# Performance work log

Measured on AMD Instinct MI355X. Metric: run time of the kernel, lower is better.

## Reference

```python
import jax, jax.numpy as jnp
import numpy as np

D_IN = 1024
D_OUT = 1024


def setup_inputs() -> dict:
    key = jax.random.key(0)
    ks = jax.random.split(key, 7)
    B, S = 4, 2048
    x = jax.random.normal(ks[0], (B, S, D_IN), dtype=jnp.float32)
    s = 1.0 / np.sqrt(D_IN)
    Wq = jax.random.uniform(ks[1], (D_IN, D_OUT), jnp.float32, -s, s)
    Wk = jax.random.uniform(ks[2], (D_IN, D_OUT), jnp.float32, -s, s)
    Wv = jax.random.uniform(ks[3], (D_IN, D_OUT), jnp.float32, -s, s)
    bq = jax.random.uniform(ks[4], (D_OUT,), jnp.float32, -s, s)
    bk = jax.random.uniform(ks[5], (D_OUT,), jnp.float32, -s, s)
    bv = jax.random.uniform(ks[6], (D_OUT,), jnp.float32, -s, s)
    return {"x": x, "Wq": Wq, "Wk": Wk, "Wv": Wv, "bq": bq, "bk": bk, "bv": bv}


def reference(x, Wq, Wk, Wv, bq, bk, bv):
    # x: [B, S, d_in]
    B, S, _ = x.shape
    q = x @ Wq + bq            # [B, S, d_out]
    k = x @ Wk + bk
    v = x @ Wv + bv
    scale = 1.0 / jnp.sqrt(jnp.asarray(q.shape[-1], q.dtype))
    scores = jnp.einsum('bqd,bkd->bqk', q, k)  # [B, S, S]
    causal = jnp.tril(jnp.ones((S, S), dtype=bool))
    scores = jnp.where(causal, scores, -jnp.inf)
    attn = jax.nn.softmax(scores * scale, axis=-1)
    return jnp.einsum('bqk,bkd->bqd', attn, v)
```

## Files before the change

### kernel.cpp

```cpp
#include <hip/hip_runtime.h>
#include <cstdint>

#define DEV __device__ __forceinline__

typedef __attribute__((ext_vector_type(4))) float f32x4;
typedef __attribute__((ext_vector_type(8))) short short8;
typedef __attribute__((ext_vector_type(4))) unsigned short u16x4;

constexpr int BS  = 4;
constexpr int SEQ = 2048;

DEV ushort f2b(float f){
  uint32_t u = __builtin_bit_cast(uint32_t, f);
  u += 0x7fffu + ((u >> 16) & 1u);
  return (ushort)(u >> 16);
}
DEV float b2f(ushort h){
  uint32_t u = (uint32_t)h << 16;
  return __builtin_bit_cast(float, u);
}

DEV void gload_lds16(const void* g, void* l){
  __builtin_amdgcn_global_load_lds(
      (const __attribute__((address_space(1))) unsigned int*)g,
      (__attribute__((address_space(3))) unsigned int*)l, 16, 0, 0);
}

#define BAR()    __builtin_amdgcn_s_barrier()
#define PRIO(x)  __builtin_amdgcn_s_setprio(x)
#define SCHEDB() __builtin_amdgcn_sched_barrier(0)
#define LGKM0()  asm volatile("s_waitcnt lgkmcnt(0)" ::: "memory")
#define WAITV(n) asm volatile("s_waitcnt vmcnt(" #n ")" ::: "memory")

__global__ __launch_bounds__(256) void convert_f2b8(const float* __restrict__ src,
                                                    ushort* __restrict__ dst){
  long i = (long)blockIdx.x * 256 + threadIdx.x;
  const f32x4* s4 = (const f32x4*)src;
  f32x4 a = s4[i*2], b = s4[i*2+1];
  short8 o;
  o[0]=(short)f2b(a[0]); o[1]=(short)f2b(a[1]); o[2]=(short)f2b(a[2]); o[3]=(short)f2b(a[3]);
  o[4]=(short)f2b(b[0]); o[5]=(short)f2b(b[1]); o[6]=(short)f2b(b[2]); o[7]=(short)f2b(b[3]);
  ((short8*)dst)[i] = o;
}

__global__ __launch_bounds__(256) void transpose_f2b(const float* __restrict__ src,
                                                     ushort* __restrict__ dst,
                                                     int R, int C){
  __shared__ float t[32][33];
  int c0 = blockIdx.x * 32, r0 = blockIdx.y * 32;
  int tx = threadIdx.x, ty = threadIdx.y;
  #pragma unroll
  for (int k=0;k<4;k++) t[ty+k*8][tx] = src[(long)(r0+ty+k*8)*C + c0+tx];
  __syncthreads();
  #pragma unroll
  for (int k=0;k<4;k++) dst[(long)(c0+ty+k*8)*R + r0+tx] = f2b(t[tx][ty+k*8]);
}

__global__ __launch_bounds__(256) void transpose_b2b(const ushort* __restrict__ src,
                                                     ushort* __restrict__ dst,
                                                     int R, int C){
  __shared__ ushort t[32][33];
  int c0 = blockIdx.x * 32, r0 = blockIdx.y * 32;
  int tx = threadIdx.x, ty = threadIdx.y;
  #pragma unroll
  for (int k=0;k<4;k++) t[ty+k*8][tx] = src[(long)(r0+ty+k*8)*C + c0+tx];
  __syncthreads();
  #pragma unroll
  for (int k=0;k<4;k++) dst[(long)(c0+ty+k*8)*R + r0+tx] = t[tx][ty+k*8];
}

struct GArgs {
  const ushort* A;  long lda; long aBS;
  const ushort* Bm; long ldb; long bBS;
  void* C;          long ldc; long cBS;
  const float* b0; const float* b1; const float* b2;
  int K;
};

template<int MODE>
__global__ __launch_bounds__(512, 2) void ring256(GArgs g){
  extern __shared__ char sm[];
  int m0, n0, z = 0;
  if (MODE == 0){
    const int fid = blockIdx.x;
    const int xcd = fid & 7, j = fid >> 3;
    m0 = (xcd * 4 + (j & 3)) * 256;
    n0 = (j >> 2) * 256;
  } else {
    m0 = blockIdx.x * 256; n0 = blockIdx.y * 256; z = blockIdx.z;
    if (n0 > m0) return;
  }
  const int tid = threadIdx.x;
  const int wid = tid >> 6, lane = tid & 63;
  const int wr = wid >> 2, wc = wid & 3;
  const int lr = lane & 15, lk = lane >> 4;

  const char* Ab = (const char*)(g.A  + (long)z * g.aBS);
  const char* Bb = (const char*)(g.Bm + (long)z * g.bBS);
  const long lda2 = g.lda * 2, ldb2 = g.ldb * 2;
  const int sr  = tid >> 2;
  const int scb = ((tid & 3) << 4) ^ (((sr >> 3) & 1) << 5);
  const char* aR0 = Ab + (long)(m0       + sr)*lda2 + scb;
  const char* aR1 = Ab + (long)(m0 + 128 + sr)*lda2 + scb;
  const char* bR0 = Bb + (long)(n0       + sr)*ldb2 + scb;
  const char* bR1 = Bb + (long)(n0 + 128 + sr)*ldb2 + scb;
  const int dst = tid << 4;

  int aoff[8], boff[4];
  #pragma unroll
  for (int m=0;m<8;m++){
    int r = wr*128 + m*16 + lr;
    aoff[m] = r*64 + ((lk*16) ^ (((r>>3)&1)<<5));
  }
  #pragma unroll
  for (int n=0;n<4;n++){
    int r = wc*64 + n*16 + lr;
    boff[n] = 16384 + r*64 + ((lk*16) ^ (((r>>3)&1)<<5));
  }

  f32x4 acc[8][4];
  #pragma unroll
  for (int m=0;m<8;m++)
    #pragma unroll
    for (int n=0;n<4;n++) acc[m][n] = f32x4{0.f,0.f,0.f,0.f};

  const int NT = g.K >> 5;
  gload_lds16(aR0,      sm + dst);
  gload_lds16(aR1,      sm + 8192  + dst);
  gload_lds16(bR0,      sm + 16384 + dst);
  gload_lds16(bR1,      sm + 24576 + dst);
  gload_lds16(aR0 + 64, sm + 32768 + dst);
  gload_lds16(aR1 + 64, sm + 32768 + 8192  + dst);
  gload_lds16(bR0 + 64, sm + 32768 + 16384 + dst);
  gload_lds16(bR1 + 64, sm + 32768 + 24576 + dst);
  WAITV(4); BAR();

  int p = 0;
  for (int t = 0; t < NT; ++t){
    const char* base = sm + p*32768;
    const int t2 = (t+2 < NT) ? t+2 : NT-1;
    const long kB = (long)(t2) << 6;
    int pS = p + 2; if (pS >= 3) pS -= 3;
    char* sb = sm + pS*32768;
    short8 af[4], bf[4];
    gload_lds16(aR0 + kB, sb + dst);
    gload_lds16(aR1 + kB, sb + 8192 + dst);
    #pragma unroll
    for (int n=0;n<4;n++) bf[n] = *(const short8*)(base + boff[n]);
    #pragma unroll
    for (int m=0;m<4;m++) af[m] = *(const short8*)(base + aoff[m]);
    LGKM0(); SCHEDB();
    PRIO(1);
    #pragma unroll
    for (int m=0;m<4;m++)
      #pragma unroll
      for (int n=0;n<4;n++)
        acc[m][n] = __builtin_amdgcn_mfma_f32_16x16x32_bf16(af[m], bf[n], acc[m][n], 0,0,0);
    PRIO(0);
    BAR();
    gload_lds16(bR0 + kB, sb + 16384 + dst);
    gload_lds16(bR1 + kB, sb + 24576 + dst);
    #pragma unroll
    for (int m=0;m<4;m++) af[m] = *(const short8*)(base + aoff[4+m]);
    LGKM0(); SCHEDB();
    PRIO(1);
    #pragma unroll
    for (int m=0;m<4;m++)
      #pragma unroll
      for (int n=0;n<4;n++)
        acc[4+m][n] = __builtin_amdgcn_mfma_f32_16x16x32_bf16(af[m], bf[n], acc[4+m][n], 0,0,0);
    PRIO(0);
    WAITV(4);
    BAR();
    p = (p+1 == 3) ? 0 : p+1;
  }
  WAITV(0);

  if (MODE == 0){
    const int sel = n0 >> 10;
    const float* bp = (sel == 0) ? g.b0 : (sel == 1) ? g.b1 : g.b2;
    ushort* Cq = (ushort*)g.C + (long)sel * 8388608;
    const int nq0 = (n0 & 1023);
    #pragma unroll
    for (int n=0;n<4;n++){
      int colq = nq0 + wc*64 + n*16 + lr;
      float bv = bp[colq];
      #pragma unroll
      for (int m=0;m<8;m++){
        int row0 = m0 + wr*128 + m*16 + lk*4;
        #pragma unroll
        for (int i=0;i<4;i++)
          Cq[(long)(row0+i)*1024 + colq] = f2b(acc[m][n][i] + bv);
      }
    }
  } else {
    ushort* Cs = (ushort*)g.C + (long)z * g.cBS;
    #pragma unroll
    for (int m=0;m<8;m++){
      int row0 = m0 + wr*128 + m*16 + lk*4;
      #pragma unroll
      for (int n=0;n<4;n++){
        int col = n0 + wc*64 + n*16 + lr;
        #pragma unroll
        for (int i=0;i<4;i++)
          Cs[(long)(row0+i)*g.ldc + col] = f2b(acc[m][n][i]);
      }
    }
  }
}

template<int MODE>
__global__ __launch_bounds__(512, 2) void gemmB(GArgs g){
  extern __shared__ char sm[];
  const int m0 = blockIdx.x * 128, n0 = blockIdx.y * 256;
  const int z  = blockIdx.z;
  const int tid = threadIdx.x;
  const int wid = tid >> 6, lane = tid & 63;
  const int wr = wid >> 2, wc = wid & 3;
  const int lr = lane & 15, lk = lane >> 4;
  const int f5 = ((lr >> 3) & 1) << 5;

  const char* Ab = (const char*)(g.A  + (long)z * g.aBS);
  const char* Bb = (const char*)(g.Bm + (long)z * g.bBS);
  const long lda2 = g.lda * 2, ldb2 = g.ldb * 2;
  const int sr  = tid >> 2;
  const int scb = ((lane & 3) << 4) ^ (((sr >> 3) & 1) << 5);
  const char* ar0 = Ab + (long)(m0 + sr)*lda2 + scb;
  const char* br0 = Bb + (long)(n0 + sr      )*ldb2 + scb;
  const char* br1 = Bb + (long)(n0 + 128 + sr)*ldb2 + scb;
  const int dwo = wid << 10;

  auto ST = [&](const char* row, int c, int off, int k0){
    const char* p = row + k0*2;
    char* d = sm + c*49152 + off + dwo;
    gload_lds16(p,      d);
    gload_lds16(p + 64, d + 8192);
  };

  const int aoffs = (wr*64 + lr)*64 + ((lk*16) ^ f5);
  const int boffs = 16384 + (wc>>1)*16384 + ((wc&1)*64 + lr)*64 + ((lk*16) ^ f5);

  f32x4 acc[4][4];
  #pragma unroll
  for (int m=0;m<4;m++)
    #pragma unroll
    for (int n=0;n<4;n++) acc[m][n] = f32x4{0.f,0.f,0.f,0.f};

  const int Keff = m0 + 128;
  const int NT = Keff >> 6;
  ST(ar0, 0, 0, 0);
  ST(br0, 0, 16384, 0); ST(br1, 0, 32768, 0);
  ST(br0, 1, 16384, 64); ST(br1, 1, 32768, 64);
  WAITV(4); BAR();

  for (int t = 0; t < NT; ++t){
    const int c = t & 1;
    const char* base = sm + c*49152;
    const int kA = ((t+1) < NT ? (t+1) : NT-1) << 6;
    const int kB = ((t+2) < NT ? (t+2) : NT-1) << 6;
    short8 bf[4][2], af[2][2];
    ST(ar0, c^1, 0, kA);
    #pragma unroll
    for (int n=0;n<4;n++)
      #pragma unroll
      for (int kk=0;kk<2;kk++)
        bf[n][kk] = *(const short8*)(base + boffs + kk*8192 + n*1024);
    #pragma unroll
    for (int mm=0;mm<2;mm++)
      #pragma unroll
      for (int kk=0;kk<2;kk++)
        af[mm][kk] = *(const short8*)(base + aoffs + kk*8192 + mm*1024);
    LGKM0(); SCHEDB();
    PRIO(1);
    #pragma unroll
    for (int kk=0;kk<2;kk++)
      #pragma unroll
      for (int mm=0;mm<2;mm++)
        #pragma unroll
        for (int n=0;n<4;n++)
          acc[mm][n] = __builtin_amdgcn_mfma_f32_16x16x32_bf16(af[mm][kk], bf[n][kk], acc[mm][n], 0,0,0);
    PRIO(0);
    BAR();
    ST(br0, c, 16384, kB); ST(br1, c, 32768, kB);
    #pragma unroll
    for (int mm=0;mm<2;mm++)
      #pragma unroll
      for (int kk=0;kk<2;kk++)
        af[mm][kk] = *(const short8*)(base + aoffs + kk*8192 + (2+mm)*1024);
    LGKM0(); SCHEDB();
    PRIO(1);
    #pragma unroll
    for (int kk=0;kk<2;kk++)
      #pragma unroll
      for (int mm=0;mm<2;mm++)
        #pragma unroll
        for (int n=0;n<4;n++)
          acc[2+mm][n] = __builtin_amdgcn_mfma_f32_16x16x32_bf16(af[mm][kk], bf[n][kk], acc[2+mm][n], 0,0,0);
    PRIO(0);
    WAITV(4);
    BAR();
  }
  WAITV(0);

  long cz = (long)z * g.cBS;
  #pragma unroll
  for (int m=0;m<4;m++){
    int row0 = m0 + wr*64 + m*16 + lk*4;
    #pragma unroll
    for (int n=0;n<4;n++){
      int col = n0 + wc*64 + n*16 + lr;
      #pragma unroll
      for (int i=0;i<4;i++)
        ((float*)g.C)[cz + (long)(row0+i)*g.ldc + col] = acc[m][n][i];
    }
  }
}

__global__ __launch_bounds__(256) void softmax_causal_b(const ushort* __restrict__ sc,
                                                        ushort* __restrict__ P){
  int row = blockIdx.x & (SEQ-1);
  int b   = blockIdx.x >> 11;
  const short8* srow = (const short8*)(sc + ((long)b*SEQ + row)*(long)SEQ);
  ushort* prow = P + ((long)b*SEQ + row)*(long)SEQ;
  int tid = threadIdx.x;
  int lane = tid & 63, wid = tid >> 6;
  const float scale = 0.03125f;
  float x[8]; float mx = -INFINITY;
  int base = tid * 8;
  if (base <= row){
    short8 v = srow[tid];
    #pragma unroll
    for (int j=0;j<8;j++){
      float t = (base + j <= row) ? b2f((ushort)v[j]) : -INFINITY;
      x[j] = t; mx = fmaxf(mx, t);
    }
  } else {
    #pragma unroll
    for (int j=0;j<8;j++) x[j] = -INFINITY;
  }
  #pragma unroll
  for (int off=1; off<64; off<<=1) mx = fmaxf(mx, __shfl_xor(mx, off));
  __shared__ float rb[8];
  if (lane == 0) rb[wid] = mx;
  __syncthreads();
  mx = fmaxf(fmaxf(rb[0],rb[1]), fmaxf(rb[2],rb[3]));
  float sum = 0.f; float e[8];
  #pragma unroll
  for (int i=0;i<8;i++){ e[i] = __expf((x[i]-mx)*scale); sum += e[i]; }
  #pragma unroll
  for (int off=1; off<64; off<<=1) sum += __shfl_xor(sum, off);
  if (lane == 0) rb[4+wid] = sum;
  __syncthreads();
  sum = (rb[4]+rb[5]) + (rb[6]+rb[7]);
  float inv = 1.0f / sum;
  int wlim = row | 127;
  if (base <= wlim){
    short8 o;
    #pragma unroll
    for (int j=0;j<8;j++) o[j] = (short)f2b(e[j]*inv);
    ((short8*)prow)[tid] = o;
  }
}

extern "C" void kernel_launch(void* const* d_in, const int* in_sizes, int n_in,
                              void* d_out, int out_size, void* d_ws, size_t ws_size,
                              hipStream_t stream){
  const float* x  = (const float*)d_in[0];
  const float* Wq = (const float*)d_in[1];
  const float* Wk = (const float*)d_in[2];
  const float* Wv = (const float*)d_in[3];
  const float* bq = (const float*)d_in[4];
  const float* bk = (const float*)d_in[5];
  const float* bv = (const float*)d_in[6];
  float* out = (float*)d_out;

  const long XB = 0;
  const long WT = 16777216;
  const long QB = 23068672;
  const long VT = 73400320;
  const long SC = 90177536;
  const long NEED = 157286400;
  const long PB = 0;
  if ((long)ws_size < NEED) return;

  char* ws = (char*)d_ws;
  ushort* xb = (ushort*)(ws + XB);
  ushort* wt = (ushort*)(ws + WT);
  ushort* qb = (ushort*)(ws + QB);
  ushort* kb = qb + 8388608;
  ushort* vb = qb + 16777216;
  ushort* vt = (ushort*)(ws + VT);
  ushort* sc = (ushort*)(ws + SC);
  ushort* pb = (ushort*)(ws + PB);

  hipFuncSetAttribute(reinterpret_cast<const void*>(&ring256<0>),
                      hipFuncAttributeMaxDynamicSharedMemorySize, 98304);
  hipFuncSetAttribute(reinterpret_cast<const void*>(&ring256<1>),
                      hipFuncAttributeMaxDynamicSharedMemorySize, 98304);
  hipFuncSetAttribute(reinterpret_cast<const void*>(&gemmB<2>),
                      hipFuncAttributeMaxDynamicSharedMemorySize, 98304);

  dim3 tb(32, 8);

  convert_f2b8<<<4096, 256, 0, stream>>>(x, xb);
  transpose_f2b<<<dim3(32,32), tb, 0, stream>>>(Wq, wt + 0,       1024, 1024);
  transpose_f2b<<<dim3(32,32), tb, 0, stream>>>(Wk, wt + 1048576, 1024, 1024);
  transpose_f2b<<<dim3(32,32), tb, 0, stream>>>(Wv, wt + 2097152, 1024, 1024);

  GArgs pa{};
  pa.A = xb; pa.lda = 1024; pa.aBS = 0;
  pa.Bm = wt; pa.ldb = 1024; pa.bBS = 0;
  pa.C = (void*)qb; pa.ldc = 1024; pa.cBS = 0;
  pa.b0 = bq; pa.b1 = bk; pa.b2 = bv;
  pa.K = 1024;
  ring256<0><<<384, 512, 98304, stream>>>(pa);

  transpose_b2b<<<dim3(32,256), tb, 0, stream>>>(vb, vt, 8192, 1024);

  GArgs sa{};
  sa.A = qb;  sa.lda = 1024; sa.aBS = (long)SEQ*1024;
  sa.Bm = kb; sa.ldb = 1024; sa.bBS = (long)SEQ*1024;
  sa.C = (void*)sc; sa.ldc = SEQ; sa.cBS = (long)SEQ*SEQ;
  sa.b0 = nullptr; sa.b1 = nullptr; sa.b2 = nullptr;
  sa.K = 1024;
  ring256<1><<<dim3(8,8,4), 512, 98304, stream>>>(sa);

  softmax_causal_b<<<BS*SEQ, 256, 0, stream>>>(sc, pb);

  GArgs va{};
  va.A = pb;  va.lda = SEQ;  va.aBS = (long)SEQ*SEQ;
  va.Bm = vt; va.ldb = 8192; va.bBS = SEQ;
  va.C = (void*)out; va.ldc = 1024; va.cBS = (long)SEQ*1024;
  va.b0 = nullptr; va.b1 = nullptr; va.b2 = nullptr;
  va.K = SEQ;
  gemmB<2><<<dim3(16,4,4), 512, 98304, stream>>>(va);
}
```

Baseline: 179.3 us.

## Restructure 256x256 GEMM into 8-phase double-buffered K=64 pipeline

Replaces the triple-buffered K=32 ring GEMM used for QKV projection and QK^T scores with a double-buffered K=64 kernel. Each iteration is split into four interleaved phases, where a quarter of the next tiles' global-to-LDS loads is issued, A fragments are read and MFMAs run. The aim is finer overlap of memory and MFMA work with fewer barriers per unit of K. LDS use rises from 96KB to 128KB per block, which may reduce the number of resident blocks per CU and adds more barriers within each iteration.

Result: no change. 178.8 us (-0.3%).

```diff
diff --git a/kernel.cpp b/kernel.cpp
--- a/kernel.cpp
+++ b/kernel.cpp
@@ -30,6 +30,7 @@
 #define PRIO(x)  __builtin_amdgcn_s_setprio(x)
 #define SCHEDB() __builtin_amdgcn_sched_barrier(0)
 #define LGKM0()  asm volatile("s_waitcnt lgkmcnt(0)" ::: "memory")
+#define LGKM8()  asm volatile("s_waitcnt lgkmcnt(8)" ::: "memory")
 #define WAITV(n) asm volatile("s_waitcnt vmcnt(" #n ")" ::: "memory")
 
 __global__ __launch_bounds__(256) void convert_f2b8(const float* __restrict__ src,
@@ -78,13 +79,13 @@
 };
 
 template<int MODE>
-__global__ __launch_bounds__(512, 2) void ring256(GArgs g){
+__global__ __launch_bounds__(512, 2) void gemm8p(GArgs g){
   extern __shared__ char sm[];
   int m0, n0, z = 0;
   if (MODE == 0){
     const int fid = blockIdx.x;
-    const int xcd = fid & 7, j = fid >> 3;
-    m0 = (xcd * 4 + (j & 3)) * 256;
+    const int j = fid >> 3;
+    m0 = ((fid & 7) * 4 + (j & 3)) * 256;
     n0 = (j >> 2) * 256;
   } else {
     m0 = blockIdx.x * 256; n0 = blockIdx.y * 256; z = blockIdx.z;
@@ -98,119 +99,130 @@
   const char* Ab = (const char*)(g.A  + (long)z * g.aBS);
   const char* Bb = (const char*)(g.Bm + (long)z * g.bBS);
   const long lda2 = g.lda * 2, ldb2 = g.ldb * 2;
-  const int sr  = tid >> 2;
-  const int scb = ((tid & 3) << 4) ^ (((sr >> 3) & 1) << 5);
-  const char* aR0 = Ab + (long)(m0       + sr)*lda2 + scb;
-  const char* aR1 = Ab + (long)(m0 + 128 + sr)*lda2 + scb;
-  const char* bR0 = Bb + (long)(n0       + sr)*ldb2 + scb;
-  const char* bR1 = Bb + (long)(n0 + 128 + sr)*ldb2 + scb;
-  const int dst = tid << 4;
+  const int srow = tid >> 2;
+  const int scol = ((tid & 3) << 4) ^ (((tid >> 5) & 1) << 5);
+  const char* sA = Ab + (long)(m0 + srow) * lda2 + scol;
+  const char* sB = Bb + (long)(n0 + srow) * ldb2 + scol;
+  const int dst16 = tid << 4;
+
+  auto STAGE = [&](int tt, int which){
+    const char* s = (which < 2)
+        ? sA + (long)(which & 1) * 128 * lda2 + (long)tt * 128
+        : sB + (long)(which & 1) * 128 * ldb2 + (long)tt * 128;
+    char* d = sm + (tt & 1) * 65536 + which * 16384 + dst16;
+    gload_lds16(s,      d);
+    gload_lds16(s + 64, d + 8192);
+  };
 
   int aoff[8], boff[4];
   #pragma unroll
-  for (int m=0;m<8;m++){
-    int r = wr*128 + m*16 + lr;
-    aoff[m] = r*64 + ((lk*16) ^ (((r>>3)&1)<<5));
-  }
-  #pragma unroll
-  for (int n=0;n<4;n++){
-    int r = wc*64 + n*16 + lr;
-    boff[n] = 16384 + r*64 + ((lk*16) ^ (((r>>3)&1)<<5));
+  for (int mm = 0; mm < 8; mm++){
+    int r = mm * 16 + lr;
+    aoff[mm] = wr * 16384 + r * 64 + ((lk * 16) ^ (((r >> 3) & 1) << 5));
+  }
+  #pragma unroll
+  for (int nn = 0; nn < 4; nn++){
+    int rb = wc * 64 + nn * 16 + lr;
+    boff[nn] = 32768 + (rb >> 7) * 16384 + (rb & 127) * 64
+             + ((lk * 16) ^ (((rb >> 3) & 1) << 5));
   }
 
   f32x4 acc[8][4];
   #pragma unroll
-  for (int m=0;m<8;m++)
-    #pragma unroll
-    for (int n=0;n<4;n++) acc[m][n] = f32x4{0.f,0.f,0.f,0.f};
-
-  const int NT = g.K >> 5;
-  gload_lds16(aR0,      sm + dst);
-  gload_lds16(aR1,      sm + 8192  + dst);
-  gload_lds16(bR0,      sm + 16384 + dst);
-  gload_lds16(bR1,      sm + 24576 + dst);
-  gload_lds16(aR0 + 64, sm + 32768 + dst);
-  gload_lds16(aR1 + 64, sm + 32768 + 8192  + dst);
-  gload_lds16(bR0 + 64, sm + 32768 + 16384 + dst);
-  gload_lds16(bR1 + 64, sm + 32768 + 24576 + dst);
+  for (int m = 0; m < 8; m++)
+    #pragma unroll
+    for (int n = 0; n < 4; n++) acc[m][n] = f32x4{0.f,0.f,0.f,0.f};
+
+  const int NT = g.K >> 6;
+  STAGE(0,2); STAGE(0,3); STAGE(0,0); STAGE(0,1);
+  STAGE(1,2); STAGE(1,3);
   WAITV(4); BAR();
 
-  int p = 0;
+  short8 af[2][2], bf[4][2];
+
+#define READ_A(MB) \
+    af[0][0] = *(const short8*)(base + aoff[MB]);            \
+    af[0][1] = *(const short8*)(base + aoff[MB] + 8192);     \
+    af[1][0] = *(const short8*)(base + aoff[MB+1]);          \
+    af[1][1] = *(const short8*)(base + aoff[MB+1] + 8192);
+#define MFMA16(MB) \
+    PRIO(1); \
+    _Pragma("unroll") \
+    for (int kk = 0; kk < 2; kk++) \
+      _Pragma("unroll") \
+      for (int mm = 0; mm < 2; mm++) \
+        _Pragma("unroll") \
+        for (int nn = 0; nn < 4; nn++) \
+          acc[MB+mm][nn] = __builtin_amdgcn_mfma_f32_16x16x32_bf16(af[mm][kk], bf[nn][kk], acc[MB+mm][nn], 0,0,0); \
+    PRIO(0);
+
   for (int t = 0; t < NT; ++t){
-    const char* base = sm + p*32768;
-    const int t2 = (t+2 < NT) ? t+2 : NT-1;
-    const long kB = (long)(t2) << 6;
-    int pS = p + 2; if (pS >= 3) pS -= 3;
-    char* sb = sm + pS*32768;
-    short8 af[4], bf[4];
-    gload_lds16(aR0 + kB, sb + dst);
-    gload_lds16(aR1 + kB, sb + 8192 + dst);
-    #pragma unroll
-    for (int n=0;n<4;n++) bf[n] = *(const short8*)(base + boff[n]);
-    #pragma unroll
-    for (int m=0;m<4;m++) af[m] = *(const short8*)(base + aoff[m]);
-    LGKM0(); SCHEDB();
-    PRIO(1);
-    #pragma unroll
-    for (int m=0;m<4;m++)
-      #pragma unroll
-      for (int n=0;n<4;n++)
-        acc[m][n] = __builtin_amdgcn_mfma_f32_16x16x32_bf16(af[m], bf[n], acc[m][n], 0,0,0);
-    PRIO(0);
-    BAR();
-    gload_lds16(bR0 + kB, sb + 16384 + dst);
-    gload_lds16(bR1 + kB, sb + 24576 + dst);
-    #pragma unroll
-    for (int m=0;m<4;m++) af[m] = *(const short8*)(base + aoff[4+m]);
-    LGKM0(); SCHEDB();
-    PRIO(1);
-    #pragma unroll
-    for (int m=0;m<4;m++)
-      #pragma unroll
-      for (int n=0;n<4;n++)
-        acc[4+m][n] = __builtin_amdgcn_mfma_f32_16x16x32_bf16(af[m], bf[n], acc[4+m][n], 0,0,0);
-    PRIO(0);
+    const char* base = sm + (t & 1) * 65536;
+    if (t + 1 < NT) STAGE(t+1, 0);
+    #pragma unroll
+    for (int nn = 0; nn < 4; nn++){
+      bf[nn][0] = *(const short8*)(base + boff[nn]);
+      bf[nn][1] = *(const short8*)(base + boff[nn] + 8192);
+    }
+    READ_A(0);
+    LGKM8();
+    SCHEDB(); BAR(); LGKM0(); SCHEDB();
+    MFMA16(0);
+    SCHEDB(); BAR();
+    if (t + 1 < NT) STAGE(t+1, 1);
+    READ_A(2);
+    SCHEDB(); BAR(); LGKM0(); SCHEDB();
+    MFMA16(2);
+    SCHEDB(); BAR();
+    if (t + 2 < NT) STAGE(t+2, 2);
+    READ_A(4);
+    SCHEDB(); BAR(); LGKM0(); SCHEDB();
+    MFMA16(4);
+    SCHEDB(); BAR();
+    if (t + 2 < NT) STAGE(t+2, 3);
+    READ_A(6);
+    SCHEDB(); BAR(); LGKM0(); SCHEDB();
+    MFMA16(6);
     WAITV(4);
-    BAR();
-    p = (p+1 == 3) ? 0 : p+1;
-  }
-  WAITV(0);
+    SCHEDB(); BAR();
+  }
+#undef READ_A
+#undef MFMA16
 
   if (MODE == 0){
     const int sel = n0 >> 10;
     const float* bp = (sel == 0) ? g.b0 : (sel == 1) ? g.b1 : g.b2;
     ushort* Cq = (ushort*)g.C + (long)sel * 8388608;
-    const int nq0 = (n0 & 1023);
-    #pragma unroll
-    for (int n=0;n<4;n++){
-      int colq = nq0 + wc*64 + n*16 + lr;
+    const int nq0 = n0 & 1023;
+    #pragma unroll
+    for (int nn = 0; nn < 4; nn++){
+      int colq = nq0 + wc*64 + nn*16 + lr;
       float bv = bp[colq];
       #pragma unroll
-      for (int m=0;m<8;m++){
-        int row0 = m0 + wr*128 + m*16 + lk*4;
+      for (int mm = 0; mm < 8; mm++){
+        int row0 = m0 + wr*128 + mm*16 + lk*4;
         #pragma unroll
-        for (int i=0;i<4;i++)
-          Cq[(long)(row0+i)*1024 + colq] = f2b(acc[m][n][i] + bv);
+        for (int i = 0; i < 4; i++)
+          Cq[(long)(row0+i)*1024 + colq] = f2b(acc[mm][nn][i] + bv);
       }
     }
   } else {
     ushort* Cs = (ushort*)g.C + (long)z * g.cBS;
     #pragma unroll
-    for (int m=0;m<8;m++){
-      int row0 = m0 + wr*128 + m*16 + lk*4;
-      #pragma unroll
-      for (int n=0;n<4;n++){
-        int col = n0 + wc*64 + n*16 + lr;
+    for (int mm = 0; mm < 8; mm++){
+      int row0 = m0 + wr*128 + mm*16 + lk*4;
+      #pragma unroll
+      for (int nn = 0; nn < 4; nn++){
+        int col = n0 + wc*64 + nn*16 + lr;
         #pragma unroll
-        for (int i=0;i<4;i++)
-          Cs[(long)(row0+i)*g.ldc + col] = f2b(acc[m][n][i]);
+        for (int i = 0; i < 4; i++)
+          Cs[(long)(row0+i)*g.ldc + col] = f2b(acc[mm][nn][i]);
       }
     }
   }
 }
 
-template<int MODE>
-__global__ __launch_bounds__(512, 2) void gemmB(GArgs g){
+__global__ __launch_bounds__(512, 2) void gemmPV(GArgs g){
   extern __shared__ char sm[];
   const int m0 = blockIdx.x * 128, n0 = blockIdx.y * 256;
   const int z  = blockIdx.z;
@@ -393,11 +405,11 @@
   ushort* sc = (ushort*)(ws + SC);
   ushort* pb = (ushort*)(ws + PB);
 
-  hipFuncSetAttribute(reinterpret_cast<const void*>(&ring256<0>),
-                      hipFuncAttributeMaxDynamicSharedMemorySize, 98304);
-  hipFuncSetAttribute(reinterpret_cast<const void*>(&ring256<1>),
-                      hipFuncAttributeMaxDynamicSharedMemorySize, 98304);
-  hipFuncSetAttribute(reinterpret_cast<const void*>(&gemmB<2>),
+  hipFuncSetAttribute(reinterpret_cast<const void*>(&gemm8p<0>),
+                      hipFuncAttributeMaxDynamicSharedMemorySize, 131072);
+  hipFuncSetAttribute(reinterpret_cast<const void*>(&gemm8p<1>),
+                      hipFuncAttributeMaxDynamicSharedMemorySize, 131072);
+  hipFuncSetAttribute(reinterpret_cast<const void*>(&gemmPV),
                       hipFuncAttributeMaxDynamicSharedMemorySize, 98304);
 
   dim3 tb(32, 8);
@@ -413,7 +425,7 @@
   pa.C = (void*)qb; pa.ldc = 1024; pa.cBS = 0;
   pa.b0 = bq; pa.b1 = bk; pa.b2 = bv;
   pa.K = 1024;
-  ring256<0><<<384, 512, 98304, stream>>>(pa);
+  gemm8p<0><<<384, 512, 131072, stream>>>(pa);
 
   transpose_b2b<<<dim3(32,256), tb, 0, stream>>>(vb, vt, 8192, 1024);
 
@@ -423,7 +435,7 @@
   sa.C = (void*)sc; sa.ldc = SEQ; sa.cBS = (long)SEQ*SEQ;
   sa.b0 = nullptr; sa.b1 = nullptr; sa.b2 = nullptr;
   sa.K = 1024;
-  ring256<1><<<dim3(8,8,4), 512, 98304, stream>>>(sa);
+  gemm8p<1><<<dim3(8,8,4), 512, 131072, stream>>>(sa);
 
   softmax_causal_b<<<BS*SEQ, 256, 0, stream>>>(sc, pb);
 
@@ -433,5 +445,5 @@
   va.C = (void*)out; va.ldc = 1024; va.cBS = (long)SEQ*1024;
   va.b0 = nullptr; va.b1 = nullptr; va.b2 = nullptr;
   va.K = SEQ;
-  gemmB<2><<<dim3(16,4,4), 512, 98304, stream>>>(va);
-}
+  gemmPV<<<dim3(16,4,4), 512, 98304, stream>>>(va);
+}
```
